# Kernel optimization log

Measured on AMD Instinct MI355X. Metric: run time of the kernel, lower is better.

The kernel has to match this reference:

```python
import jax, jax.numpy as jnp
import numpy as np

D_MODEL = 1024
NUM_HEADS = 16
MAX_SEQ_LEN = 2048
THETA = 10000.0
D_K = D_MODEL // NUM_HEADS


def setup_inputs() -> dict:
    key = jax.random.key(0)
    ks = jax.random.split(key, 5)
    x = jax.random.normal(ks[0], (2, 2048, D_MODEL), dtype=jnp.float32)
    token_positions = jnp.arange(2048, dtype=jnp.int32)
    s = 1.0 / np.sqrt(D_MODEL)
    w_q = jax.random.normal(ks[1], (D_MODEL, D_MODEL), dtype=jnp.float32) * s
    w_k = jax.random.normal(ks[2], (D_MODEL, D_MODEL), dtype=jnp.float32) * s
    w_v = jax.random.normal(ks[3], (D_MODEL, D_MODEL), dtype=jnp.float32) * s
    w_o = jax.random.normal(ks[4], (D_MODEL, D_MODEL), dtype=jnp.float32) * s
    return {"x": x, "token_positions": token_positions,
            "w_q": w_q, "w_k": w_k, "w_v": w_v, "w_o": w_o}


def _rope_tables():
    inv_freq = 1.0 / (THETA ** (jnp.arange(0, D_K, 2, dtype=jnp.float32) / D_K))
    angles = jnp.arange(MAX_SEQ_LEN, dtype=jnp.float32)[:, None] * inv_freq[None, :]
    return jnp.cos(angles), jnp.sin(angles)  # [max_seq_len, d_k//2]


def _apply_rope(x, cos, sin):
    # x: [..., s, d_k]; interleaved-pair rotation, cos/sin: [s, d_k//2]
    x0 = x[..., 0::2]
    x1 = x[..., 1::2]
    y0 = x0 * cos - x1 * sin
    y1 = x0 * sin + x1 * cos
    return jnp.stack((y0, y1), axis=-1).reshape(x.shape)


def reference(x, token_positions, w_q, w_k, w_v, w_o):
    b, s, _ = x.shape
    h, dk = NUM_HEADS, D_K
    # torch Linear: y = x @ W^T
    q = (x @ w_q.T).reshape(b, s, h, dk).transpose(0, 2, 1, 3)  # [b,h,s,dk]
    k = (x @ w_k.T).reshape(b, s, h, dk).transpose(0, 2, 1, 3)
    v = (x @ w_v.T).reshape(b, s, h, dk).transpose(0, 2, 1, 3)
    cos_c, sin_c = _rope_tables()
    cos = cos_c[token_positions]  # [s, dk//2]
    sin = sin_c[token_positions]
    q = _apply_rope(q, cos, sin)
    k = _apply_rope(k, cos, sin)
    scores = jnp.einsum('bhqd,bhkd->bhqk', q, k) / jnp.sqrt(jnp.float32(dk))
    causal = jnp.tril(jnp.ones((s, s), dtype=bool))
    scores = jnp.where(causal, scores, -jnp.inf)
    attn = jax.nn.softmax(scores, axis=-1)
    out = jnp.einsum('bhqk,bhkd->bhqd', attn, v)
    out = out.transpose(0, 2, 1, 3).reshape(b, s, h * dk)
    return out @ w_o.T
```

## Files before the change

### kernel.cpp

```cpp
#include <hip/hip_runtime.h>
#include <cstdint>
#include <cstddef>

#define DEV static __device__ __forceinline__

typedef __attribute__((ext_vector_type(8))) short bf16x8;
typedef __attribute__((ext_vector_type(4))) float f32x4;

DEV uint16_t f2bf(float f) {
  uint32_t u = __builtin_bit_cast(uint32_t, f);
  u += 0x7FFFu + ((u >> 16) & 1u);
  return (uint16_t)(u >> 16);
}

DEV uint16_t f2bf_trunc(float f) {
  return (uint16_t)(__builtin_bit_cast(uint32_t, f) >> 16);
}

DEV float fexp2(float x) { return __builtin_amdgcn_exp2f(x); }

template <int CTRL>
DEV float dppf(float v) {
  return __builtin_bit_cast(
      float, __builtin_amdgcn_update_dpp(0, __builtin_bit_cast(int, v), CTRL, 0xF, 0xF, true));
}
DEV float rowmax16(float v) {
  v = fmaxf(v, dppf<0xB1>(v));
  v = fmaxf(v, dppf<0x4E>(v));
  v = fmaxf(v, dppf<0x124>(v));
  v = fmaxf(v, dppf<0x128>(v));
  return v;
}
DEV float rowsum16(float v) {
  v += dppf<0xB1>(v);
  v += dppf<0x4E>(v);
  v += dppf<0x124>(v);
  v += dppf<0x128>(v);
  return v;
}

DEV void load_lds16(const void* g, void* l) {
  auto gp = reinterpret_cast<const uint32_t __attribute__((address_space(1)))*>(
      reinterpret_cast<uintptr_t>(g));
  auto lp = reinterpret_cast<uint32_t __attribute__((address_space(3)))*>(
      reinterpret_cast<uintptr_t>(l));
  __builtin_amdgcn_global_load_lds(gp, lp, 16, 0, 0);
}

__global__ __launch_bounds__(256) void cvt_all(const float* __restrict__ x,
                                               const float* __restrict__ wq,
                                               const float* __restrict__ wk,
                                               const float* __restrict__ wv,
                                               const float* __restrict__ wo,
                                               const int* __restrict__ tokpos,
                                               uint16_t* __restrict__ dst,
                                               float2* __restrict__ rtab) {
  int bx = blockIdx.x;
  if (bx >= 8192) {
    int idx = (bx - 8192) * 256 + threadIdx.x;
    int s = idx >> 5, f = idx & 31;
    float invf = __expf(-0.28782314f * (float)f);
    float pos = (float)tokpos[s];
    float sn, cs;
    __sincosf(pos * invf, &sn, &cs);
    rtab[idx] = make_float2(cs, sn);
    return;
  }
  int gi = bx * 1024 + threadIdx.x * 4;
  const float* s;
  int li;
  if (gi < 4194304) {
    s = x; li = gi;
  } else {
    int j = gi - 4194304;
    int r = j >> 20;
    li = j & 1048575;
    s = (r == 0) ? wq : (r == 1) ? wk : (r == 2) ? wv : wo;
  }
  float4 v = *reinterpret_cast<const float4*>(s + li);
  ushort4 o;
  o.x = f2bf(v.x); o.y = f2bf(v.y); o.z = f2bf(v.z); o.w = f2bf(v.w);
  *reinterpret_cast<ushort4*>(dst + gi) = o;
}

__global__ __launch_bounds__(256) void gemm_qkv(const uint16_t* __restrict__ A,
                                                const uint16_t* __restrict__ Wqkv,
                                                uint16_t* __restrict__ QK,
                                                uint16_t* __restrict__ VTb,
                                                const float2* __restrict__ rtab) {
  __shared__ union {
    struct { uint16_t a[128 * 64]; uint16_t b[128 * 64]; } st;
    uint16_t t[128 * 128];
  } sm;

  const int tid = threadIdx.x;
  const int lane = tid & 63, w = tid >> 6;
  const int q = lane >> 4, l16 = lane & 15;
  const int wm = w & 1, wn = w >> 1;
  const int bm = blockIdx.y, bn = blockIdx.x;
  const int wsel = bn >> 3;

  const f32x4 z4 = {0.f, 0.f, 0.f, 0.f};
  f32x4 acc[4][4];
#pragma unroll
  for (int i = 0; i < 4; ++i)
#pragma unroll
    for (int j = 0; j < 4; ++j) acc[i][j] = z4;

  const int srow = tid >> 3, sslot = tid & 7;
  const uint16_t* Ab = A + (size_t)bm * 128 * 1024;
  const uint16_t* Bb = Wqkv + (size_t)bn * 128 * 1024;

  for (int k0 = 0; k0 < 1024; k0 += 64) {
    __syncthreads();
#pragma unroll
    for (int is = 0; is < 4; ++is) {
      int row = is * 32 + srow;
      int gch = sslot ^ (row & 7);
      char* la = (char*)sm.st.a + (is * 32 + w * 8) * 128;
      char* lb = (char*)sm.st.b + (is * 32 + w * 8) * 128;
      load_lds16(Ab + (size_t)row * 1024 + k0 + gch * 8, la);
      load_lds16(Bb + (size_t)row * 1024 + k0 + gch * 8, lb);
    }
    __syncthreads();
#pragma unroll
    for (int ks = 0; ks < 2; ++ks) {
      bf16x8 af[4], bfr[4];
#pragma unroll
      for (int i = 0; i < 4; ++i) {
        int ra = wm * 64 + i * 16 + l16;
        af[i] = *reinterpret_cast<const bf16x8*>(sm.st.a + ra * 64 +
                                                 (((ks * 4 + q) ^ (ra & 7)) * 8));
        int rb = wn * 64 + i * 16 + l16;
        bfr[i] = *reinterpret_cast<const bf16x8*>(sm.st.b + rb * 64 +
                                                  (((ks * 4 + q) ^ (rb & 7)) * 8));
      }
#pragma unroll
      for (int i = 0; i < 4; ++i)
#pragma unroll
        for (int j = 0; j < 4; ++j)
          acc[i][j] =
              __builtin_amdgcn_mfma_f32_16x16x32_bf16(af[i], bfr[j], acc[i][j], 0, 0, 0);
    }
  }

  if (wsel < 2) {
    uint16_t* O = QK + (size_t)wsel * 4194304;
    const float scq = (wsel == 0) ? 0.18033688f : 1.0f;
#pragma unroll
    for (int j = 0; j < 4; ++j) {
      int gn = bn * 128 + wn * 64 + j * 16 + l16;
      int cn = gn & 1023;
      int f = (gn & 63) >> 1;
      float sgn = (lane & 1) ? 1.f : -1.f;
#pragma unroll
      for (int i = 0; i < 4; ++i) {
#pragma unroll
        for (int r = 0; r < 4; ++r) {
          int gm = bm * 128 + wm * 64 + i * 16 + q * 4 + r;
          float2 cssn = rtab[(gm & 2047) * 32 + f];
          float v = acc[i][j][r];
          float o = dppf<0xB1>(v);
          O[(size_t)gm * 1024 + cn] = f2bf((v * cssn.x + sgn * o * cssn.y) * scq);
        }
      }
    }
  } else {
    const int bnv = bn & 7;
    __syncthreads();
#pragma unroll
    for (int i = 0; i < 4; ++i)
#pragma unroll
      for (int j = 0; j < 4; ++j)
#pragma unroll
        for (int r = 0; r < 4; ++r) {
          int mL = wm * 64 + i * 16 + q * 4 + r;
          int nL = wn * 64 + j * 16 + l16;
          int ch = (mL >> 3) ^ (nL & 15);
          sm.t[nL * 128 + ch * 8 + (mL & 7)] = f2bf(acc[i][j][r]);
        }
    __syncthreads();
    const int b = (bm * 128) >> 11;
    const int sblk = (bm * 128) & 2047;
#pragma unroll
    for (int it = 0; it < 8; ++it) {
      int nL = it * 16 + (tid >> 4);
      int mch = tid & 15;
      int slot = mch ^ (nL & 15);
      bf16x8 vv = *reinterpret_cast<const bf16x8*>(sm.t + nL * 128 + slot * 8);
      int gn = bnv * 128 + nL;
      int h = gn >> 6, d = gn & 63;
      *reinterpret_cast<bf16x8*>(VTb + ((size_t)((b * 16 + h) * 64 + d)) * 2048 + sblk +
                                 mch * 8) = vv;
    }
  }
}

__global__ __launch_bounds__(256) void gemm_out(const uint16_t* __restrict__ A,
                                                const uint16_t* __restrict__ Bw,
                                                float* __restrict__ O) {
  __shared__ uint16_t sa[128 * 64];
  __shared__ uint16_t sb[64 * 64];

  const int tid = threadIdx.x;
  const int lane = tid & 63, w = tid >> 6;
  const int q = lane >> 4, l16 = lane & 15;
  const int bm = blockIdx.y, bn = blockIdx.x;

  const f32x4 z4 = {0.f, 0.f, 0.f, 0.f};
  f32x4 acc[2][4];
#pragma unroll
  for (int i = 0; i < 2; ++i)
#pragma unroll
    for (int j = 0; j < 4; ++j) acc[i][j] = z4;

  const int srow = tid >> 3, sslot = tid & 7;
  const uint16_t* Ab = A + (size_t)bm * 128 * 1024;
  const uint16_t* Bb = Bw + (size_t)bn * 64 * 1024;

  for (int k0 = 0; k0 < 1024; k0 += 64) {
    __syncthreads();
#pragma unroll
    for (int is = 0; is < 4; ++is) {
      int row = is * 32 + srow;
      int gch = sslot ^ (row & 7);
      load_lds16(Ab + (size_t)row * 1024 + k0 + gch * 8,
                 (char*)sa + (is * 32 + w * 8) * 128);
    }
#pragma unroll
    for (int is = 0; is < 2; ++is) {
      int row = is * 32 + srow;
      int gch = sslot ^ (row & 7);
      load_lds16(Bb + (size_t)row * 1024 + k0 + gch * 8,
                 (char*)sb + (is * 32 + w * 8) * 128);
    }
    __syncthreads();
#pragma unroll
    for (int ks = 0; ks < 2; ++ks) {
      bf16x8 af[2], bfr[4];
#pragma unroll
      for (int i = 0; i < 2; ++i) {
        int ra = w * 32 + i * 16 + l16;
        af[i] = *reinterpret_cast<const bf16x8*>(sa + ra * 64 +
                                                 (((ks * 4 + q) ^ (ra & 7)) * 8));
      }
#pragma unroll
      for (int j = 0; j < 4; ++j) {
        int rb = j * 16 + l16;
        bfr[j] = *reinterpret_cast<const bf16x8*>(sb + rb * 64 +
                                                  (((ks * 4 + q) ^ (rb & 7)) * 8));
      }
#pragma unroll
      for (int i = 0; i < 2; ++i)
#pragma unroll
        for (int j = 0; j < 4; ++j)
          acc[i][j] =
              __builtin_amdgcn_mfma_f32_16x16x32_bf16(af[i], bfr[j], acc[i][j], 0, 0, 0);
    }
  }

#pragma unroll
  for (int i = 0; i < 2; ++i)
#pragma unroll
    for (int r = 0; r < 4; ++r) {
      int gm = bm * 128 + w * 32 + i * 16 + q * 4 + r;
#pragma unroll
      for (int j = 0; j < 4; ++j) {
        int gn = bn * 64 + j * 16 + l16;
        O[(size_t)gm * 1024 + gn] = acc[i][j][r];
      }
    }
}

__global__ __launch_bounds__(256) void flash_attn(const uint16_t* __restrict__ Q,
                                                  const uint16_t* __restrict__ K,
                                                  const uint16_t* __restrict__ VT,
                                                  uint16_t* __restrict__ AO) {
  __shared__ uint16_t ksm[2][128 * 64];
  __shared__ uint16_t vsm[2][64 * 128];
  __shared__ uint16_t psm[4][32 * 128];

  const int tid = threadIdx.x;
  const int lane = tid & 63, w = tid >> 6;
  const int q = lane >> 4, l16 = lane & 15;
  const int p = blockIdx.x;
  const int bh = blockIdx.y;
  const int b = bh >> 4, h = bh & 15;

  const size_t baseBS = (size_t)b * 2048 * 1024 + h * 64;
  const size_t baseVT = (size_t)bh * 64 * 2048;
  uint16_t* pw = psm[w];
  const f32x4 z4 = {0.f, 0.f, 0.f, 0.f};

  auto stage = [&](int buf, int kt) {
#pragma unroll
    for (int is = 0; is < 4; ++is) {
      int row = is * 32 + (tid >> 3);
      int gch = (tid & 7) ^ (row & 7);
      load_lds16(K + baseBS + (size_t)(kt * 128 + row) * 1024 + gch * 8,
                 (char*)ksm[buf] + (is * 32 + w * 8) * 128);
    }
#pragma unroll
    for (int is = 0; is < 4; ++is) {
      int row = is * 16 + (tid >> 4);
      int gch = (tid & 15) ^ (row & 15);
      load_lds16(VT + baseVT + (size_t)row * 2048 + kt * 128 + gch * 8,
                 (char*)vsm[buf] + (is * 16 + w * 4) * 256);
    }
  };

  for (int t = 0; t < 2; ++t) {
    const int qt = t ? (15 - p) : p;
    const int r0 = qt * 128 + w * 32;
    const int nkt = qt + 1;

    bf16x8 qf[2][2];
#pragma unroll
    for (int mi = 0; mi < 2; ++mi)
#pragma unroll
      for (int ks = 0; ks < 2; ++ks)
        qf[mi][ks] = *reinterpret_cast<const bf16x8*>(
            Q + baseBS + (size_t)(r0 + mi * 16 + l16) * 1024 + ks * 32 + q * 8);

    f32x4 oa[2][4];
#pragma unroll
    for (int mi = 0; mi < 2; ++mi)
#pragma unroll
      for (int di = 0; di < 4; ++di) oa[mi][di] = z4;
    float m2[2][4], li[2][4];
#pragma unroll
    for (int mi = 0; mi < 2; ++mi)
#pragma unroll
      for (int r = 0; r < 4; ++r) { m2[mi][r] = -1e30f; li[mi][r] = 0.f; }

    __syncthreads();
    stage(0, 0);

    for (int kt = 0; kt < nkt; ++kt) {
      const int cur = kt & 1;
      __syncthreads();
      if (kt + 1 < nkt) stage(cur ^ 1, kt + 1);

      f32x4 sc[2][8];
#pragma unroll
      for (int mi = 0; mi < 2; ++mi)
#pragma unroll
        for (int nj = 0; nj < 8; ++nj) sc[mi][nj] = z4;
#pragma unroll
      for (int ks = 0; ks < 2; ++ks) {
        bf16x8 kf[8];
#pragma unroll
        for (int nj = 0; nj < 8; ++nj) {
          int rk = nj * 16 + l16;
          kf[nj] = *reinterpret_cast<const bf16x8*>(ksm[cur] + rk * 64 +
                                                    (((ks * 4 + q) ^ (rk & 7)) * 8));
        }
#pragma unroll
        for (int mi = 0; mi < 2; ++mi)
#pragma unroll
          for (int nj = 0; nj < 8; ++nj)
            sc[mi][nj] =
                __builtin_amdgcn_mfma_f32_16x16x32_bf16(qf[mi][ks], kf[nj], sc[mi][nj], 0, 0, 0);
      }

      if (kt == nkt - 1) {
#pragma unroll
        for (int mi = 0; mi < 2; ++mi)
#pragma unroll
          for (int nj = 0; nj < 8; ++nj)
#pragma unroll
            for (int r = 0; r < 4; ++r) {
              int col = kt * 128 + nj * 16 + l16;
              int row = r0 + mi * 16 + q * 4 + r;
              if (col > row) sc[mi][nj][r] = -1e30f;
            }
      }

      float alpha[2][4];
#pragma unroll
      for (int mi = 0; mi < 2; ++mi)
#pragma unroll
        for (int r = 0; r < 4; ++r) {
          float v = fmaxf(
              fmaxf(fmaxf(sc[mi][0][r], sc[mi][1][r]), fmaxf(sc[mi][2][r], sc[mi][3][r])),
              fmaxf(fmaxf(sc[mi][4][r], sc[mi][5][r]), fmaxf(sc[mi][6][r], sc[mi][7][r])));
          v = rowmax16(v);
          float mn = fmaxf(m2[mi][r], v);
          alpha[mi][r] = fexp2(m2[mi][r] - mn);
          m2[mi][r] = mn;
          li[mi][r] *= alpha[mi][r];
        }

#pragma unroll
      for (int mi = 0; mi < 2; ++mi)
#pragma unroll
        for (int nj = 0; nj < 8; ++nj)
#pragma unroll
          for (int r = 0; r < 4; ++r) {
            float pv = fexp2(sc[mi][nj][r] - m2[mi][r]);
            li[mi][r] += pv;
            int pr = mi * 16 + q * 4 + r;
            int pc = nj * 16 + l16;
            pw[pr * 128 + (((pc >> 3) ^ (pr & 15)) * 8) + (pc & 7)] = f2bf_trunc(pv);
          }

#pragma unroll
      for (int mi = 0; mi < 2; ++mi)
#pragma unroll
        for (int di = 0; di < 4; ++di)
#pragma unroll
          for (int r = 0; r < 4; ++r) oa[mi][di][r] *= alpha[mi][r];

#pragma unroll
      for (int ks = 0; ks < 4; ++ks) {
        bf16x8 pf[2];
#pragma unroll
        for (int mi = 0; mi < 2; ++mi) {
          int pr = mi * 16 + l16;
          pf[mi] = *reinterpret_cast<const bf16x8*>(pw + pr * 128 +
                                                    (((ks * 4 + q) ^ (pr & 15)) * 8));
        }
        bf16x8 vf[4];
#pragma unroll
        for (int di = 0; di < 4; ++di) {
          int vr = di * 16 + l16;
          vf[di] = *reinterpret_cast<const bf16x8*>(vsm[cur] + vr * 128 +
                                                    (((ks * 4 + q) ^ (vr & 15)) * 8));
        }
#pragma unroll
        for (int mi = 0; mi < 2; ++mi)
#pragma unroll
          for (int di = 0; di < 4; ++di)
            oa[mi][di] =
                __builtin_amdgcn_mfma_f32_16x16x32_bf16(pf[mi], vf[di], oa[mi][di], 0, 0, 0);
      }
    }

#pragma unroll
    for (int mi = 0; mi < 2; ++mi)
#pragma unroll
      for (int r = 0; r < 4; ++r) {
        float inv = 1.f / rowsum16(li[mi][r]);
        int gm = r0 + mi * 16 + q * 4 + r;
#pragma unroll
        for (int di = 0; di < 4; ++di)
          AO[baseBS + (size_t)gm * 1024 + di * 16 + l16] = f2bf(oa[mi][di][r] * inv);
      }
  }
}

extern "C" void kernel_launch(void* const* d_in, const int* in_sizes, int n_in,
                              void* d_out, int out_size, void* d_ws, size_t ws_size,
                              hipStream_t stream) {
  (void)in_sizes; (void)n_in; (void)out_size; (void)ws_size;
  const float* x = (const float*)d_in[0];
  const int* tokpos = (const int*)d_in[1];
  const float* wq = (const float*)d_in[2];
  const float* wk = (const float*)d_in[3];
  const float* wv = (const float*)d_in[4];
  const float* wo = (const float*)d_in[5];
  float* out = (float*)d_out;

  uint16_t* ws = (uint16_t*)d_ws;
  uint16_t* xb = ws;
  uint16_t* wqb = xb + 4194304;
  uint16_t* wob = wqb + 3145728;
  uint16_t* Qb = wob + 1048576;
  uint16_t* VTb = Qb + 8388608;
  uint16_t* AOb = VTb + 4194304;
  float2* rtab = (float2*)AOb;

  cvt_all<<<8448, 256, 0, stream>>>(x, wq, wk, wv, wo, tokpos, xb, rtab);

  gemm_qkv<<<dim3(24, 32), 256, 0, stream>>>(xb, wqb, Qb, VTb, rtab);

  flash_attn<<<dim3(8, 32), 256, 0, stream>>>(Qb, Qb + 4194304, VTb, AOb);

  gemm_out<<<dim3(16, 32), 256, 0, stream>>>(AOb, wob, out);
}
```

Measured before the change: 194.6 us.

## Split flash-attention query tile across 8 waves of 16 rows each

```diff
diff --git a/kernel.cpp b/kernel.cpp
--- a/kernel.cpp
+++ b/kernel.cpp
@@ -272,13 +272,13 @@
     }
 }
 
-__global__ __launch_bounds__(256) void flash_attn(const uint16_t* __restrict__ Q,
+__global__ __launch_bounds__(512) void flash_attn(const uint16_t* __restrict__ Q,
                                                   const uint16_t* __restrict__ K,
                                                   const uint16_t* __restrict__ VT,
                                                   uint16_t* __restrict__ AO) {
   __shared__ uint16_t ksm[2][128 * 64];
   __shared__ uint16_t vsm[2][64 * 128];
-  __shared__ uint16_t psm[4][32 * 128];
+  __shared__ uint16_t psm[8][16 * 128];
 
   const int tid = threadIdx.x;
   const int lane = tid & 63, w = tid >> 6;
@@ -294,44 +294,38 @@
 
   auto stage = [&](int buf, int kt) {
 #pragma unroll
-    for (int is = 0; is < 4; ++is) {
-      int row = is * 32 + (tid >> 3);
+    for (int is = 0; is < 2; ++is) {
+      int row = is * 64 + (tid >> 3);
       int gch = (tid & 7) ^ (row & 7);
       load_lds16(K + baseBS + (size_t)(kt * 128 + row) * 1024 + gch * 8,
-                 (char*)ksm[buf] + (is * 32 + w * 8) * 128);
-    }
-#pragma unroll
-    for (int is = 0; is < 4; ++is) {
-      int row = is * 16 + (tid >> 4);
+                 (char*)ksm[buf] + (is * 64 + w * 8) * 128);
+    }
+#pragma unroll
+    for (int is = 0; is < 2; ++is) {
+      int row = is * 32 + (tid >> 4);
       int gch = (tid & 15) ^ (row & 15);
       load_lds16(VT + baseVT + (size_t)row * 2048 + kt * 128 + gch * 8,
-                 (char*)vsm[buf] + (is * 16 + w * 4) * 256);
+                 (char*)vsm[buf] + (is * 32 + w * 4) * 256);
     }
   };
 
   for (int t = 0; t < 2; ++t) {
     const int qt = t ? (15 - p) : p;
-    const int r0 = qt * 128 + w * 32;
+    const int r0 = qt * 128 + w * 16;
     const int nkt = qt + 1;
 
-    bf16x8 qf[2][2];
-#pragma unroll
-    for (int mi = 0; mi < 2; ++mi)
-#pragma unroll
-      for (int ks = 0; ks < 2; ++ks)
-        qf[mi][ks] = *reinterpret_cast<const bf16x8*>(
-            Q + baseBS + (size_t)(r0 + mi * 16 + l16) * 1024 + ks * 32 + q * 8);
-
-    f32x4 oa[2][4];
-#pragma unroll
-    for (int mi = 0; mi < 2; ++mi)
-#pragma unroll
-      for (int di = 0; di < 4; ++di) oa[mi][di] = z4;
-    float m2[2][4], li[2][4];
-#pragma unroll
-    for (int mi = 0; mi < 2; ++mi)
-#pragma unroll
-      for (int r = 0; r < 4; ++r) { m2[mi][r] = -1e30f; li[mi][r] = 0.f; }
+    bf16x8 qf[2];
+#pragma unroll
+    for (int ks = 0; ks < 2; ++ks)
+      qf[ks] = *reinterpret_cast<const bf16x8*>(
+          Q + baseBS + (size_t)(r0 + l16) * 1024 + ks * 32 + q * 8);
+
+    f32x4 oa[4];
+#pragma unroll
+    for (int di = 0; di < 4; ++di) oa[di] = z4;
+    float m2[4], li[4];
+#pragma unroll
+    for (int r = 0; r < 4; ++r) { m2[r] = -1e30f; li[r] = 0.f; }
 
     __syncthreads();
     stage(0, 0);
@@ -341,11 +335,9 @@
       __syncthreads();
       if (kt + 1 < nkt) stage(cur ^ 1, kt + 1);
 
-      f32x4 sc[2][8];
-#pragma unroll
-      for (int mi = 0; mi < 2; ++mi)
-#pragma unroll
-        for (int nj = 0; nj < 8; ++nj) sc[mi][nj] = z4;
+      f32x4 sc[8];
+#pragma unroll
+      for (int nj = 0; nj < 8; ++nj) sc[nj] = z4;
 #pragma unroll
       for (int ks = 0; ks < 2; ++ks) {
         bf16x8 kf[8];
@@ -356,69 +348,58 @@
                                                     (((ks * 4 + q) ^ (rk & 7)) * 8));
         }
 #pragma unroll
-        for (int mi = 0; mi < 2; ++mi)
-#pragma unroll
-          for (int nj = 0; nj < 8; ++nj)
-            sc[mi][nj] =
-                __builtin_amdgcn_mfma_f32_16x16x32_bf16(qf[mi][ks], kf[nj], sc[mi][nj], 0, 0, 0);
+        for (int nj = 0; nj < 8; ++nj)
+          sc[nj] =
+              __builtin_amdgcn_mfma_f32_16x16x32_bf16(qf[ks], kf[nj], sc[nj], 0, 0, 0);
       }
 
       if (kt == nkt - 1) {
 #pragma unroll
-        for (int mi = 0; mi < 2; ++mi)
-#pragma unroll
-          for (int nj = 0; nj < 8; ++nj)
-#pragma unroll
-            for (int r = 0; r < 4; ++r) {
-              int col = kt * 128 + nj * 16 + l16;
-              int row = r0 + mi * 16 + q * 4 + r;
-              if (col > row) sc[mi][nj][r] = -1e30f;
-            }
-      }
-
-      float alpha[2][4];
-#pragma unroll
-      for (int mi = 0; mi < 2; ++mi)
+        for (int nj = 0; nj < 8; ++nj)
+#pragma unroll
+          for (int r = 0; r < 4; ++r) {
+            int col = kt * 128 + nj * 16 + l16;
+            int row = r0 + q * 4 + r;
+            if (col > row) sc[nj][r] = -1e30f;
+          }
+      }
+
+      float alpha[4];
+#pragma unroll
+      for (int r = 0; r < 4; ++r) {
+        float v = fmaxf(
+            fmaxf(fmaxf(sc[0][r], sc[1][r]), fmaxf(sc[2][r], sc[3][r])),
+            fmaxf(fmaxf(sc[4][r], sc[5][r]), fmaxf(sc[6][r], sc[7][r])));
+        v = rowmax16(v);
+        float mn = fmaxf(m2[r], v);
+        alpha[r] = fexp2(m2[r] - mn);
+        m2[r] = mn;
+        li[r] *= alpha[r];
+      }
+
+#pragma unroll
+      for (int nj = 0; nj < 8; ++nj)
 #pragma unroll
         for (int r = 0; r < 4; ++r) {
-          float v = fmaxf(
-              fmaxf(fmaxf(sc[mi][0][r], sc[mi][1][r]), fmaxf(sc[mi][2][r], sc[mi][3][r])),
-              fmaxf(fmaxf(sc[mi][4][r], sc[mi][5][r]), fmaxf(sc[mi][6][r], sc[mi][7][r])));
-          v = rowmax16(v);
-          float mn = fmaxf(m2[mi][r], v);
-          alpha[mi][r] = fexp2(m2[mi][r] - mn);
-          m2[mi][r] = mn;
-          li[mi][r] *= alpha[mi][r];
-        }
-
-#pragma unroll
-      for (int mi = 0; mi < 2; ++mi)
-#pragma unroll
-        for (int nj = 0; nj < 8; ++nj)
-#pragma unroll
-          for (int r = 0; r < 4; ++r) {
-            float pv = fexp2(sc[mi][nj][r] - m2[mi][r]);
-            li[mi][r] += pv;
-            int pr = mi * 16 + q * 4 + r;
-            int pc = nj * 16 + l16;
-            pw[pr * 128 + (((pc >> 3) ^ (pr & 15)) * 8) + (pc & 7)] = f2bf_trunc(pv);
-          }
-
-#pragma unroll
-      for (int mi = 0; mi < 2; ++mi)
-#pragma unroll
-        for (int di = 0; di < 4; ++di)
-#pragma unroll
-          for (int r = 0; r < 4; ++r) oa[mi][di][r] *= alpha[mi][r];
+          float pv = fexp2(sc[nj][r] - m2[r]);
+          li[r] += pv;
+          int pr = q * 4 + r;
+          int pc = nj * 16 + l16;
+          pw[pr * 128 + (((pc >> 3) ^ (pr & 15)) * 8) + (pc & 7)] = f2bf_trunc(pv);
+        }
+
+#pragma unroll
+      for (int di = 0; di < 4; ++di)
+#pragma unroll
+        for (int r = 0; r < 4; ++r) oa[di][r] *= alpha[r];
 
 #pragma unroll
       for (int ks = 0; ks < 4; ++ks) {
-        bf16x8 pf[2];
-#pragma unroll
-        for (int mi = 0; mi < 2; ++mi) {
-          int pr = mi * 16 + l16;
-          pf[mi] = *reinterpret_cast<const bf16x8*>(pw + pr * 128 +
-                                                    (((ks * 4 + q) ^ (pr & 15)) * 8));
+        bf16x8 pf;
+        {
+          int pr = l16;
+          pf = *reinterpret_cast<const bf16x8*>(pw + pr * 128 +
+                                                (((ks * 4 + q) ^ (pr & 15)) * 8));
         }
         bf16x8 vf[4];
 #pragma unroll
@@ -428,24 +409,20 @@
                                                     (((ks * 4 + q) ^ (vr & 15)) * 8));
         }
 #pragma unroll
-        for (int mi = 0; mi < 2; ++mi)
-#pragma unroll
-          for (int di = 0; di < 4; ++di)
-            oa[mi][di] =
-                __builtin_amdgcn_mfma_f32_16x16x32_bf16(pf[mi], vf[di], oa[mi][di], 0, 0, 0);
-      }
-    }
-
-#pragma unroll
-    for (int mi = 0; mi < 2; ++mi)
-#pragma unroll
-      for (int r = 0; r < 4; ++r) {
-        float inv = 1.f / rowsum16(li[mi][r]);
-        int gm = r0 + mi * 16 + q * 4 + r;
-#pragma unroll
         for (int di = 0; di < 4; ++di)
-          AO[baseBS + (size_t)gm * 1024 + di * 16 + l16] = f2bf(oa[mi][di][r] * inv);
-      }
+          oa[di] =
+              __builtin_amdgcn_mfma_f32_16x16x32_bf16(pf, vf[di], oa[di], 0, 0, 0);
+      }
+    }
+
+#pragma unroll
+    for (int r = 0; r < 4; ++r) {
+      float inv = 1.f / rowsum16(li[r]);
+      int gm = r0 + q * 4 + r;
+#pragma unroll
+      for (int di = 0; di < 4; ++di)
+        AO[baseBS + (size_t)gm * 1024 + di * 16 + l16] = f2bf(oa[di][r] * inv);
+    }
   }
 }
 
@@ -474,7 +451,7 @@
 
   gemm_qkv<<<dim3(24, 32), 256, 0, stream>>>(xb, wqb, Qb, VTb, rtab);
 
-  flash_attn<<<dim3(8, 32), 256, 0, stream>>>(Qb, Qb + 4194304, VTb, AOb);
+  flash_attn<<<dim3(8, 32), 512, 0, stream>>>(Qb, Qb + 4194304, VTb, AOb);
 
   gemm_out<<<dim3(16, 32), 256, 0, stream>>>(AOb, wob, out);
 }
```

Measured after the change: 185.3 us. 1.05x faster.
